# Kernel tuning notes

Hardware: AMD Instinct MI355X
Metric: run time of the kernel (lower is better)

The kernel has to match this reference:

```python
import jax, jax.numpy as jnp
import numpy as np

V_IPC, N_ROLES, D = 50000, 16, 256
B, L = 2048, 64
F_BIB, H1, H2, D_OUT = 512, 1024, 1024, 512
N_EXP, N_CLS = 8, 10
LN_EPS = 1e-5


def setup_inputs() -> dict:
    key = jax.random.key(0)
    ks = jax.random.split(key, 24)
    s = 0.05
    ipc_emb = jax.random.normal(ks[0], (V_IPC, D), jnp.float32) * s
    ipc_emb = ipc_emb.at[0].set(0.0)  # padding_idx=0
    role_emb = jax.random.normal(ks[1], (N_ROLES, D), jnp.float32) * s
    role_emb = role_emb.at[0].set(0.0)
    inp = {
        "ipc_indices": jax.random.randint(ks[2], (B, L), 0, V_IPC),
        "role_indices": jax.random.randint(ks[3], (B, L), 0, N_ROLES),
        "bibliometric_features": jax.random.normal(ks[4], (B, F_BIB), jnp.float32),
        "ipc_padding_mask": jax.random.randint(ks[5], (B, L), 0, 2).astype(jnp.int32),
        "top_k": 2,
        "ipc_emb": ipc_emb,
        "role_emb": role_emb,
        "Wq": jax.random.normal(ks[6], (D, D), jnp.float32) * s,
        "bq": jnp.zeros((D,), jnp.float32),
        "Wk": jax.random.normal(ks[7], (D, D), jnp.float32) * s,
        "bk": jnp.zeros((D,), jnp.float32),
        "Wv": jax.random.normal(ks[8], (D, D), jnp.float32) * s,
        "bv": jnp.zeros((D,), jnp.float32),
        "global_context": jax.random.normal(ks[9], (D,), jnp.float32) * s,
        "ln_g": jnp.ones((D,), jnp.float32),
        "ln_b": jnp.zeros((D,), jnp.float32),
        "gate_W": jax.random.normal(ks[10], (D, N_EXP), jnp.float32) * s,
        "gate_b": jnp.zeros((N_EXP,), jnp.float32),
        "expert_biases": jnp.zeros((N_EXP,), jnp.float32),
        "W1": jax.random.normal(ks[11], (N_EXP, F_BIB, H1), jnp.float32) * s,
        "b1": jnp.zeros((N_EXP, H1), jnp.float32),
        "W2": jax.random.normal(ks[12], (N_EXP, H1, H2), jnp.float32) * s,
        "b2": jnp.zeros((N_EXP, H2), jnp.float32),
        "W3": jax.random.normal(ks[13], (N_EXP, H2, D_OUT), jnp.float32) * s,
        "b3": jnp.zeros((N_EXP, D_OUT), jnp.float32),
        "head_W": jax.random.normal(ks[14], (D_OUT, N_CLS), jnp.float32) * s,
        "head_b": jnp.zeros((N_CLS,), jnp.float32),
    }
    return inp


def reference(ipc_indices, role_indices, bibliometric_features, ipc_padding_mask, top_k,
              ipc_emb, role_emb, Wq, bq, Wk, bk, Wv, bv, global_context, ln_g, ln_b,
              gate_W, gate_b, expert_biases, W1, b1, W2, b2, W3, b3, head_W, head_b):
    # embeddings + role combine  -> [B, L, D]
    x = ipc_emb[ipc_indices] + role_emb[role_indices]
    # attention pooling with a global learned query (same query for every batch row)
    keys = x @ Wk + bk                                  # [B, L, D]
    values = x @ Wv + bv                                # [B, L, D]
    q = global_context @ Wq + bq                        # [D]
    scores = jnp.einsum('d,bld->bl', q, keys)           # [B, L]
    scores = jnp.where(ipc_padding_mask == 0, -1e9, scores)
    attn = jax.nn.softmax(scores, axis=-1)              # [B, L]
    pooled = jnp.einsum('bl,bld->bd', attn, values)     # [B, D]
    mu = pooled.mean(-1, keepdims=True)
    var = ((pooled - mu) ** 2).mean(-1, keepdims=True)
    router_in = (pooled - mu) / jnp.sqrt(var + LN_EPS) * ln_g + ln_b
    # router: select with biased scores, gate with unbiased scores
    affinity = router_in @ gate_W + gate_b              # [B, E]
    sel_scores = affinity + expert_biases
    _, idx = jax.lax.top_k(sel_scores, top_k)           # [B, K]
    gw = jax.nn.softmax(jnp.take_along_axis(affinity, idx, axis=-1), axis=-1)  # [B, K]
    # dense all-expert MLP (reference form of masked per-expert loop)
    h = jax.nn.relu(jnp.einsum('bi,eih->ebh', bibliometric_features, W1) + b1[:, None, :])
    h = jax.nn.relu(jnp.einsum('ebh,ehj->ebj', h, W2) + b2[:, None, :])
    eo = jnp.einsum('ebj,ejo->ebo', h, W3) + b3[:, None, :]  # [E, B, O]
    # gather each token's top-k expert outputs and combine
    bidx = jnp.arange(idx.shape[0])[:, None]            # [B, 1]
    sel_out = eo[idx, bidx]                             # [B, K, O]
    moe_out = jnp.einsum('bk,bko->bo', gw, sel_out)     # [B, O]
    logits = moe_out @ head_W + head_b                  # [B, n_classes]
    return logits, idx
```

## Files before the change

### kernel.cpp

```cpp
#include <hip/hip_runtime.h>
#include <hip/hip_bf16.h>
#include <math.h>


#define LN_EPS 1e-5f

typedef __bf16 bf16_t;
typedef __bf16 bf16x8 __attribute__((ext_vector_type(8)));
typedef float f32x4 __attribute__((ext_vector_type(4)));

struct f4x2 { float4 a, b; };
__device__ __forceinline__ f4x2 ldA8(const float* p) {
  f4x2 v; v.a = *(const float4*)p; v.b = *(const float4*)(p + 4); return v;
}
__device__ __forceinline__ bf16x8 cvt8(const f4x2& v) {
  bf16x8 o;
  o[0] = (bf16_t)v.a.x; o[1] = (bf16_t)v.a.y; o[2] = (bf16_t)v.a.z; o[3] = (bf16_t)v.a.w;
  o[4] = (bf16_t)v.b.x; o[5] = (bf16_t)v.b.y; o[6] = (bf16_t)v.b.z; o[7] = (bf16_t)v.b.w;
  return o;
}

__global__ __launch_bounds__(256)
void transpose_prep(const float* __restrict__ W1, const float* __restrict__ W2,
                    const float* __restrict__ W3, bf16_t* __restrict__ B1,
                    bf16_t* __restrict__ B2, bf16_t* __restrict__ B3,
                    const float* __restrict__ Wq, const float* __restrict__ bq,
                    const float* __restrict__ Wk, const float* __restrict__ bk,
                    const float* __restrict__ gc, float* __restrict__ kq_out) {
  __shared__ float tile[64][65];
  const int z = blockIdx.z;
  if (z == 24) {
    if (blockIdx.y >= 2) return;
    float* q = &tile[0][0];
    float* red = &tile[0][0] + 256;
    const int t = threadIdx.x, bi = blockIdx.y * 16 + blockIdx.x;
    float s = bq[t];
    for (int d = 0; d < 256; d++) s += gc[d] * Wq[d * 256 + t];
    q[t] = s;
    __syncthreads();
    const int rl = t >> 5, sl = t & 31;
    const int r = bi * 8 + rl;
    float p = 0.f;
#pragma unroll
    for (int i = 0; i < 8; i++) { const int d = sl + 32 * i; p += Wk[r * 256 + d] * q[d]; }
#pragma unroll
    for (int o = 16; o > 0; o >>= 1) p += __shfl_down(p, o, 32);
    if (sl == 0) kq_out[r] = p;
    if (bi == 0) {
      float z2 = q[t] * bk[t];
      const int lane = t & 63, wave = t >> 6;
#pragma unroll
      for (int o = 32; o > 0; o >>= 1) z2 += __shfl_down(z2, o);
      if (lane == 0) red[wave] = z2;
      __syncthreads();
      if (t == 0) kq_out[256] = red[0] + red[1] + red[2] + red[3];
    }
    return;
  }
  const float* W; bf16_t* Bft; int K, N, e;
  if (z < 8)       { W = W1; Bft = B1; K = 512;  N = 1024; e = z; }
  else if (z < 16) { W = W2; Bft = B2; K = 1024; N = 1024; e = z - 8; }
  else             { W = W3; Bft = B3; K = 1024; N = 512;  e = z - 16; }
  const int n0 = blockIdx.x * 64, k0 = blockIdx.y * 64;
  if (n0 >= N || k0 >= K) return;
  const float* Wp = W + (size_t)e * K * N;
  bf16_t* Bp = Bft + (size_t)e * N * K;
  const int tq = threadIdx.x & 15, th = threadIdx.x >> 4;
#pragma unroll
  for (int i = 0; i < 4; i++) {
    const int row = th + 16 * i;
    *(float4*)&tile[row][tq * 4] = *(const float4*)(Wp + (size_t)(k0 + row) * N + n0 + tq * 4);
  }
  __syncthreads();
  const int lane = threadIdx.x & 63, sub = threadIdx.x >> 6;
  const int nk = K >> 5;
#pragma unroll
  for (int it = 0; it < 2; it++) {
    const int fid = sub + it * 4;
    const int ntl = fid & 3, ktl = fid >> 2;
    const int n_l = ntl * 16 + (lane & 15);
    const int k_l = ktl * 32 + (lane >> 4) * 8;
    bf16x8 o;
#pragma unroll
    for (int j = 0; j < 8; j++) o[j] = (bf16_t)tile[k_l + j][n_l];
    const size_t idx = ((((size_t)(n0 >> 4) + ntl) * nk + (k0 >> 5) + ktl) * 64 + lane) * 8;
    *(bf16x8*)(Bp + idx) = o;
  }
}

__global__ __launch_bounds__(256)
void score_tab_kernel(const float* __restrict__ ipc_emb,
                      const float* __restrict__ role_emb,
                      const float* __restrict__ kq_qbk, float* __restrict__ tab) {
  const int wave = threadIdx.x >> 6, lane = threadIdx.x & 63;
  const float4 kq = *(const float4*)(kq_qbk + lane * 4);
  const int base = (blockIdx.x * 4 + wave) * 32;
  for (int i = 0; i < 32; i++) {
    const int r = base + i;
    if (r >= 50016) return;
    const float* src = (r < 50000) ? (ipc_emb + (size_t)r * 256)
                                   : (role_emb + (size_t)(r - 50000) * 256);
    const float4 v = *(const float4*)(src + lane * 4);
    float p = v.x * kq.x + v.y * kq.y + v.z * kq.z + v.w * kq.w;
#pragma unroll
    for (int o = 32; o > 0; o >>= 1) p += __shfl_down(p, o);
    if (lane == 0) tab[r] = (r < 50000) ? p : (p + kq_qbk[256]);
  }
}

__global__ __launch_bounds__(256)
void xbar_kernel(const int* __restrict__ ipc_idx, const int* __restrict__ role_idx,
                 const int* __restrict__ maskp,
                 const float* __restrict__ ipc_emb, const float* __restrict__ role_emb,
                 const float* __restrict__ tab, float* __restrict__ xbar_g) {
  const int b = blockIdx.x;
  __shared__ float attn_s[64];
  __shared__ __align__(16) float part[4][256];
  const int t = threadIdx.x, wave = t >> 6, lane = t & 63;
  const int d0 = lane * 4;
  if (wave == 0) {
    const int ii = ipc_idx[b * 64 + lane], ri = role_idx[b * 64 + lane];
    float s = tab[ii] + tab[50000 + ri];
    s = (maskp[b * 64 + lane] == 0) ? -1e9f : s;
    float m = s;
#pragma unroll
    for (int o = 32; o > 0; o >>= 1) m = fmaxf(m, __shfl_xor(m, o));
    const float ev = expf(s - m);
    float sum = ev;
#pragma unroll
    for (int o = 32; o > 0; o >>= 1) sum += __shfl_xor(sum, o);
    attn_s[lane] = ev / sum;
  }
  __syncthreads();
  float p0 = 0.f, p1 = 0.f, p2 = 0.f, p3 = 0.f;
  for (int l = wave; l < 64; l += 4) {
    const float a = attn_s[l];
    if (a == 0.f) continue;
    const int ii = ipc_idx[b * 64 + l], ri = role_idx[b * 64 + l];
    const float4 xe = *(const float4*)(ipc_emb + (size_t)ii * 256 + d0);
    const float4 re = *(const float4*)(role_emb + (size_t)ri * 256 + d0);
    p0 += a * (xe.x + re.x); p1 += a * (xe.y + re.y);
    p2 += a * (xe.z + re.z); p3 += a * (xe.w + re.w);
  }
  *(float4*)&part[wave][d0] = make_float4(p0, p1, p2, p3);
  __syncthreads();
  xbar_g[(size_t)b * 256 + t] = part[0][t] + part[1][t] + part[2][t] + part[3][t];
}

__global__ __launch_bounds__(256)
void pool_kernel(const float* __restrict__ xbar_g, const float* __restrict__ Wv,
                 const float* __restrict__ bvec,
                 const float* __restrict__ ln_g, const float* __restrict__ ln_b,
                 const float* __restrict__ gate_W, const float* __restrict__ gate_b,
                 const float* __restrict__ expert_biases,
                 float* __restrict__ out_idx_f, int* __restrict__ ws_idx,
                 float* __restrict__ ws_gw) {
  const int rb = blockIdx.x * 8;
  __shared__ __align__(16) float xs[8][256];
  __shared__ __align__(16) float ps[8][260];
  const int t = threadIdx.x, wave = t >> 6, lane = t & 63;
  for (int i = t; i < 512; i += 256)
    ((float4*)xs)[i] = ((const float4*)(xbar_g + (size_t)rb * 256))[i];
  __syncthreads();
  const float* x0 = xs[wave * 2];
  const float* x1 = xs[wave * 2 + 1];
  f32x4 acc0 = {0.f, 0.f, 0.f, 0.f}, acc1 = {0.f, 0.f, 0.f, 0.f};
  for (int d = 0; d < 256; d += 4) {
    const float4 xa = *(const float4*)(x0 + d);
    const float4 xb = *(const float4*)(x1 + d);
#pragma unroll
    for (int j = 0; j < 4; j++) {
      const float4 wv = *(const float4*)(Wv + (size_t)(d + j) * 256 + lane * 4);
      const float aj = (&xa.x)[j], bj = (&xb.x)[j];
      acc0.x += aj * wv.x; acc0.y += aj * wv.y; acc0.z += aj * wv.z; acc0.w += aj * wv.w;
      acc1.x += bj * wv.x; acc1.y += bj * wv.y; acc1.z += bj * wv.z; acc1.w += bj * wv.w;
    }
  }
  const float4 bvv = *(const float4*)(bvec + lane * 4);
  acc0.x += bvv.x; acc0.y += bvv.y; acc0.z += bvv.z; acc0.w += bvv.w;
  acc1.x += bvv.x; acc1.y += bvv.y; acc1.z += bvv.z; acc1.w += bvv.w;
  *(f32x4*)&ps[wave * 2][lane * 4] = acc0;
  *(f32x4*)&ps[wave * 2 + 1][lane * 4] = acc1;
  __syncthreads();
  const float4 lg = *(const float4*)(ln_g + lane * 4);
  const float4 lb = *(const float4*)(ln_b + lane * 4);
#pragma unroll
  for (int rr = 0; rr < 2; rr++) {
    const int r = wave * 2 + rr;
    const float4 v = *(const float4*)&ps[r][lane * 4];
    float s1 = v.x + v.y + v.z + v.w;
#pragma unroll
    for (int o = 32; o > 0; o >>= 1) s1 += __shfl_xor(s1, o);
    const float mu = s1 * (1.f / 256.f);
    const float4 df = make_float4(v.x - mu, v.y - mu, v.z - mu, v.w - mu);
    float s2 = df.x * df.x + df.y * df.y + df.z * df.z + df.w * df.w;
#pragma unroll
    for (int o = 32; o > 0; o >>= 1) s2 += __shfl_xor(s2, o);
    const float inv = 1.f / sqrtf(s2 * (1.f / 256.f) + LN_EPS);
    f32x4 rv;
    rv[0] = df.x * inv * lg.x + lb.x; rv[1] = df.y * inv * lg.y + lb.y;
    rv[2] = df.z * inv * lg.z + lb.z; rv[3] = df.w * inv * lg.w + lb.w;
    f32x4 pa = {0.f, 0.f, 0.f, 0.f}, pb = {0.f, 0.f, 0.f, 0.f};
#pragma unroll
    for (int k = 0; k < 4; k++) {
      const int d = lane * 4 + k;
      const f32x4 g0 = *(const f32x4*)(gate_W + d * 8);
      const f32x4 g1 = *(const f32x4*)(gate_W + d * 8 + 4);
      pa += rv[k] * g0;
      pb += rv[k] * g1;
    }
#pragma unroll
    for (int o = 32; o > 0; o >>= 1) {
      pa[0] += __shfl_down(pa[0], o); pa[1] += __shfl_down(pa[1], o);
      pa[2] += __shfl_down(pa[2], o); pa[3] += __shfl_down(pa[3], o);
      pb[0] += __shfl_down(pb[0], o); pb[1] += __shfl_down(pb[1], o);
      pb[2] += __shfl_down(pb[2], o); pb[3] += __shfl_down(pb[3], o);
    }
    if (lane == 0) {
      float aff[8];
#pragma unroll
      for (int j = 0; j < 4; j++) { aff[j] = pa[j] + gate_b[j]; aff[4 + j] = pb[j] + gate_b[4 + j]; }
      float b0 = -1e30f; int i0 = 0;
#pragma unroll
      for (int j = 0; j < 8; j++) {
        const float s = aff[j] + expert_biases[j];
        if (s > b0) { b0 = s; i0 = j; }
      }
      float b1v = -1e30f; int i1 = 0;
#pragma unroll
      for (int j = 0; j < 8; j++) {
        const float s = aff[j] + expert_biases[j];
        if (j != i0 && s > b1v) { b1v = s; i1 = j; }
      }
      const float a0 = aff[i0], a1 = aff[i1];
      const float m = fmaxf(a0, a1);
      const float e0 = expf(a0 - m), e1 = expf(a1 - m);
      const float invs = 1.f / (e0 + e1);
      const int bg = rb + r;
      ws_idx[bg * 2] = i0; ws_idx[bg * 2 + 1] = i1;
      ws_gw[bg * 2] = e0 * invs; ws_gw[bg * 2 + 1] = e1 * invs;
      out_idx_f[bg * 2] = (float)i0; out_idx_f[bg * 2 + 1] = (float)i1;
    }
  }
}

__global__ __launch_bounds__(256)
void pack_kernel(const int* __restrict__ ws_idx, int* __restrict__ list_token,
                 int* __restrict__ a_of, int* __restrict__ offsets_g) {
  __shared__ int cnt[8]; __shared__ int off[9]; __shared__ int fill[8];
  const int t = threadIdx.x;
  if (t < 8) cnt[t] = 0;
  __syncthreads();
  for (int a = t; a < 4096; a += 256) atomicAdd(&cnt[ws_idx[a]], 1);
  __syncthreads();
  if (t == 0) {
    off[0] = 0;
    for (int e = 0; e < 8; e++) off[e + 1] = off[e] + ((cnt[e] + 63) & ~63);
  }
  __syncthreads();
  if (t < 8) fill[t] = off[t];
  if (t < 9) offsets_g[t] = off[t];
  for (int a = t; a < 4608; a += 256) list_token[a] = 0;
  __syncthreads();
  for (int a = t; a < 4096; a += 256) {
    const int e = ws_idx[a];
    const int pos = atomicAdd(&fill[e], 1);
    list_token[pos] = a >> 1;
    a_of[a] = pos;
  }
}

template <int NT, bool RELU>
__global__ __launch_bounds__(256)
void expert_gemm_g1(const float* __restrict__ bib, const int* __restrict__ list_token,
                    const bf16_t* __restrict__ Bft, const float* __restrict__ bias,
                    bf16_t* __restrict__ C, const int* __restrict__ offsets) {
  constexpr int K = 512, nk = K / 32;
  const int e = blockIdx.z;
  const int seg_hi = offsets[e + 1];
  const int blk_row = offsets[e] + blockIdx.y * 128;
  if (blk_row >= seg_hi) return;
  const int wave = threadIdx.x >> 6, lane = threadIdx.x & 63;
  const int row0 = blk_row + wave * 32;
  if (row0 >= seg_hi) return;
  const int n0 = blockIdx.x * 64;
  const int tok0 = list_token[row0 + (lane & 15)];
  const int tok1 = list_token[row0 + 16 + (lane & 15)];
  const float* Ap0 = bib + (size_t)tok0 * 512 + (lane >> 4) * 8;
  const float* Ap1 = bib + (size_t)tok1 * 512 + (lane >> 4) * 8;
  const bf16_t* Bp = Bft + (size_t)e * NT * K + ((size_t)(n0 >> 4) * nk * 512 + lane * 8);
  f32x4 acc[2][4];
#pragma unroll
  for (int i = 0; i < 2; i++)
#pragma unroll
    for (int j = 0; j < 4; j++) acc[i][j] = (f32x4){0.f, 0.f, 0.f, 0.f};
  f4x2 aS[2][2]; bf16x8 bX[2][4];
  aS[0][0] = ldA8(Ap0); aS[0][1] = ldA8(Ap1);
#pragma unroll
  for (int ni = 0; ni < 4; ni++) bX[0][ni] = *(const bf16x8*)(Bp + (size_t)ni * nk * 512);
#pragma unroll
  for (int kt = 0; kt < nk; kt++) {
    const int cur = kt & 1, nxt = cur ^ 1;
    if (kt + 1 < nk) {
      aS[nxt][0] = ldA8(Ap0 + (kt + 1) * 32);
      aS[nxt][1] = ldA8(Ap1 + (kt + 1) * 32);
#pragma unroll
      for (int ni = 0; ni < 4; ni++)
        bX[nxt][ni] = *(const bf16x8*)(Bp + ((size_t)ni * nk + kt + 1) * 512);
    }
    const bf16x8 a0 = cvt8(aS[cur][0]), a1 = cvt8(aS[cur][1]);
#pragma unroll
    for (int ni = 0; ni < 4; ni++) {
      acc[0][ni] = __builtin_amdgcn_mfma_f32_16x16x32_bf16(a0, bX[cur][ni], acc[0][ni], 0, 0, 0);
      acc[1][ni] = __builtin_amdgcn_mfma_f32_16x16x32_bf16(a1, bX[cur][ni], acc[1][ni], 0, 0, 0);
    }
  }
  const int fr = lane & 15, q = lane >> 4;
#pragma unroll
  for (int ni = 0; ni < 4; ni++) {
    const int col = n0 + ni * 16 + fr;
    const float bv = bias[e * NT + col];
#pragma unroll
    for (int mi = 0; mi < 2; mi++) {
#pragma unroll
      for (int r = 0; r < 4; r++) {
        const int row = row0 + mi * 16 + q * 4 + r;
        float v = acc[mi][ni][r] + bv;
        if (RELU) v = fmaxf(v, 0.f);
        C[(size_t)row * NT + col] = (bf16_t)v;
      }
    }
  }
}

template <int K, int NT, bool RELU, typename OUT_T>
__global__ __launch_bounds__(256)
void expert_gemm_ft(const bf16_t* __restrict__ A, const bf16_t* __restrict__ Bft,
                    const float* __restrict__ bias, OUT_T* __restrict__ C,
                    const int* __restrict__ offsets) {
  constexpr int nk = K / 32;
  const int e = blockIdx.z;
  const int seg_hi = offsets[e + 1];
  const int blk_row = offsets[e] + blockIdx.y * 128;
  if (blk_row >= seg_hi) return;
  const int wave = threadIdx.x >> 6, lane = threadIdx.x & 63;
  const int row0 = blk_row + wave * 32;
  if (row0 >= seg_hi) return;
  const int n0 = blockIdx.x * 64;
  const bf16_t* Ap = A + (size_t)(row0 + (lane & 15)) * K + ((lane >> 4) * 8);
  const bf16_t* Bp = Bft + (size_t)e * NT * K + ((size_t)(n0 >> 4) * nk * 512 + lane * 8);
  f32x4 acc[2][4];
#pragma unroll
  for (int i = 0; i < 2; i++)
#pragma unroll
    for (int j = 0; j < 4; j++) acc[i][j] = (f32x4){0.f, 0.f, 0.f, 0.f};
  bf16x8 aX[2][2], bX[2][4];
#pragma unroll
  for (int mi = 0; mi < 2; mi++) aX[0][mi] = *(const bf16x8*)(Ap + mi * 16 * K);
#pragma unroll
  for (int ni = 0; ni < 4; ni++) bX[0][ni] = *(const bf16x8*)(Bp + (size_t)ni * nk * 512);
#pragma unroll
  for (int kt = 0; kt < nk; kt++) {
    const int cur = kt & 1, nxt = cur ^ 1;
    if (kt + 1 < nk) {
#pragma unroll
      for (int mi = 0; mi < 2; mi++)
        aX[nxt][mi] = *(const bf16x8*)(Ap + mi * 16 * K + (kt + 1) * 32);
#pragma unroll
      for (int ni = 0; ni < 4; ni++)
        bX[nxt][ni] = *(const bf16x8*)(Bp + ((size_t)ni * nk + kt + 1) * 512);
    }
#pragma unroll
    for (int mi = 0; mi < 2; mi++)
#pragma unroll
      for (int ni = 0; ni < 4; ni++)
        acc[mi][ni] = __builtin_amdgcn_mfma_f32_16x16x32_bf16(aX[cur][mi], bX[cur][ni], acc[mi][ni], 0, 0, 0);
  }
  const int fr = lane & 15, q = lane >> 4;
#pragma unroll
  for (int ni = 0; ni < 4; ni++) {
    const int col = n0 + ni * 16 + fr;
    const float bv = bias[e * NT + col];
#pragma unroll
    for (int mi = 0; mi < 2; mi++) {
#pragma unroll
      for (int r = 0; r < 4; r++) {
        const int row = row0 + mi * 16 + q * 4 + r;
        float v = acc[mi][ni][r] + bv;
        if (RELU) v = fmaxf(v, 0.f);
        C[(size_t)row * NT + col] = (OUT_T)v;
      }
    }
  }
}

__global__ __launch_bounds__(256)
void head_kernel(const float* __restrict__ O, const int* __restrict__ a_of,
                 const float* __restrict__ ws_gw, const float* __restrict__ head_W,
                 const float* __restrict__ head_b, float* __restrict__ out) {
  const int b = blockIdx.x, t = threadIdx.x;
  __shared__ float m[512];
  const int a0 = a_of[b * 2], a1 = a_of[b * 2 + 1];
  const float g0 = ws_gw[b * 2], g1 = ws_gw[b * 2 + 1];
  for (int d = t; d < 512; d += 256)
    m[d] = g0 * O[(size_t)a0 * 512 + d] + g1 * O[(size_t)a1 * 512 + d];
  __syncthreads();
  if (t < 160) {
    const int c = t >> 4, ch = t & 15;
    float p = 0.f;
#pragma unroll
    for (int i = 0; i < 32; i++) {
      const int d = i * 16 + ch;
      p += m[d] * head_W[d * 10 + c];
    }
#pragma unroll
    for (int o = 8; o > 0; o >>= 1) p += __shfl_down(p, o, 16);
    if (ch == 0) out[b * 10 + c] = p + head_b[c];
  }
}

extern "C" void kernel_launch(void* const* d_in, const int* in_sizes, int n_in,
                              void* d_out, int out_size, void* d_ws, size_t ws_size,
                              hipStream_t stream) {
  const int* ipc_idx = (const int*)d_in[0];
  const int* role_idx = (const int*)d_in[1];
  const float* bib = (const float*)d_in[2];
  const int* maskp = (const int*)d_in[3];
  const float* ipc_emb = (const float*)d_in[5];
  const float* role_emb = (const float*)d_in[6];
  const float* Wq = (const float*)d_in[7];
  const float* bq = (const float*)d_in[8];
  const float* Wk = (const float*)d_in[9];
  const float* bk = (const float*)d_in[10];
  const float* Wv = (const float*)d_in[11];
  const float* bv = (const float*)d_in[12];
  const float* gc = (const float*)d_in[13];
  const float* ln_g = (const float*)d_in[14];
  const float* ln_b = (const float*)d_in[15];
  const float* gate_W = (const float*)d_in[16];
  const float* gate_b = (const float*)d_in[17];
  const float* exp_b = (const float*)d_in[18];
  const float* W1 = (const float*)d_in[19];
  const float* b1 = (const float*)d_in[20];
  const float* W2 = (const float*)d_in[21];
  const float* b2 = (const float*)d_in[22];
  const float* W3 = (const float*)d_in[23];
  const float* b3 = (const float*)d_in[24];
  const float* head_W = (const float*)d_in[25];
  const float* head_b = (const float*)d_in[26];

  char* ws = (char*)d_ws;
  size_t off = 0;
  auto alloc = [&](size_t bytes) -> char* {
    char* p = ws + off;
    off += (bytes + 255) & ~(size_t)255;
    return p;
  };
  float* kq_qbk = (float*)alloc(257 * 4);
  float* tab = (float*)alloc(50016 * 4);
  float* xbar_g = (float*)alloc((size_t)2048 * 256 * 4);
  int* ws_idx = (int*)alloc(4096 * 4);
  float* ws_gw = (float*)alloc(4096 * 4);
  int* list_tok = (int*)alloc(4608 * 4);
  int* a_of = (int*)alloc(4096 * 4);
  int* offs = (int*)alloc(9 * 4);
  bf16_t* W1t = (bf16_t*)alloc((size_t)8 * 1024 * 512 * 2);
  bf16_t* W2t = (bf16_t*)alloc((size_t)8 * 1024 * 1024 * 2);
  bf16_t* W3t = (bf16_t*)alloc((size_t)8 * 512 * 1024 * 2);
  bf16_t* H1c = (bf16_t*)alloc((size_t)4608 * 1024 * 2);
  bf16_t* H2c = (bf16_t*)alloc((size_t)4608 * 1024 * 2);
  float* Oc = (float*)alloc((size_t)4608 * 512 * 4);
  (void)in_sizes; (void)n_in; (void)out_size; (void)ws_size;

  float* out_logits = (float*)d_out;
  float* out_idx = (float*)d_out + 20480;

  transpose_prep<<<dim3(16, 16, 25), 256, 0, stream>>>(W1, W2, W3, W1t, W2t, W3t,
                                                       Wq, bq, Wk, bk, gc, kq_qbk);
  score_tab_kernel<<<391, 256, 0, stream>>>(ipc_emb, role_emb, kq_qbk, tab);
  xbar_kernel<<<2048, 256, 0, stream>>>(ipc_idx, role_idx, maskp, ipc_emb, role_emb,
                                        tab, xbar_g);
  pool_kernel<<<256, 256, 0, stream>>>(xbar_g, Wv, bv, ln_g, ln_b, gate_W, gate_b,
                                       exp_b, out_idx, ws_idx, ws_gw);
  pack_kernel<<<1, 256, 0, stream>>>(ws_idx, list_tok, a_of, offs);
  expert_gemm_g1<1024, true><<<dim3(16, 36, 8), 256, 0, stream>>>(bib, list_tok, W1t, b1, H1c, offs);
  expert_gemm_ft<1024, 1024, true, bf16_t><<<dim3(16, 36, 8), 256, 0, stream>>>(H1c, W2t, b2, H2c, offs);
  expert_gemm_ft<1024, 512, false, float><<<dim3(8, 36, 8), 256, 0, stream>>>(H2c, W3t, b3, Oc, offs);
  head_kernel<<<2048, 256, 0, stream>>>(Oc, a_of, ws_gw, head_W, head_b, out_logits);
}
```

Measured before the change: 379.7 us.

## Fold W3 into head weights, dropping the third expert GEMM

Since the last expert layer is linear and is followed directly by the linear head, W3·head_W and b3·head_W are precomputed per expert in the prep kernel, giving a 1024x10 matrix per expert. The head kernel then reads H2 rows directly and applies the folded weights. This removes the 1024x512 expert GEMM and the fp32 Oc intermediate. In exchange, the prep kernel recomputes the folded weights on every call, and the last layer now runs in fp32 from bf16 H2 rather than through a bf16 GEMM, which changes rounding slightly.

```diff
diff --git a/kernel.cpp b/kernel.cpp
--- a/kernel.cpp
+++ b/kernel.cpp
@@ -22,57 +22,106 @@
 
 __global__ __launch_bounds__(256)
 void transpose_prep(const float* __restrict__ W1, const float* __restrict__ W2,
-                    const float* __restrict__ W3, bf16_t* __restrict__ B1,
-                    bf16_t* __restrict__ B2, bf16_t* __restrict__ B3,
+                    bf16_t* __restrict__ B1, bf16_t* __restrict__ B2,
                     const float* __restrict__ Wq, const float* __restrict__ bq,
                     const float* __restrict__ Wk, const float* __restrict__ bk,
-                    const float* __restrict__ gc, float* __restrict__ kq_out) {
+                    const float* __restrict__ gc, float* __restrict__ kq_out,
+                    const float* __restrict__ W3, const float* __restrict__ head_W,
+                    const float* __restrict__ b3, float* __restrict__ W3hT,
+                    float* __restrict__ b3h) {
   __shared__ float tile[64][65];
   const int z = blockIdx.z;
-  if (z == 24) {
-    if (blockIdx.y >= 2) return;
-    float* q = &tile[0][0];
-    float* red = &tile[0][0] + 256;
-    const int t = threadIdx.x, bi = blockIdx.y * 16 + blockIdx.x;
-    float s = bq[t];
-    for (int d = 0; d < 256; d++) s += gc[d] * Wq[d * 256 + t];
-    q[t] = s;
+  const int t = threadIdx.x;
+  if (z == 16) {
+    if (blockIdx.y < 2) {
+      float* q = &tile[0][0];
+      float* red = &tile[0][0] + 256;
+      const int bi = blockIdx.y * 16 + blockIdx.x;
+      float s = bq[t];
+      for (int d = 0; d < 256; d++) s += gc[d] * Wq[d * 256 + t];
+      q[t] = s;
+      __syncthreads();
+      const int rl = t >> 5, sl = t & 31;
+      const int r = bi * 8 + rl;
+      float p = 0.f;
+#pragma unroll
+      for (int i = 0; i < 8; i++) { const int d = sl + 32 * i; p += Wk[r * 256 + d] * q[d]; }
+#pragma unroll
+      for (int o = 16; o > 0; o >>= 1) p += __shfl_down(p, o, 32);
+      if (sl == 0) kq_out[r] = p;
+      if (bi == 0) {
+        float z2 = q[t] * bk[t];
+        const int lane = t & 63, wave = t >> 6;
+#pragma unroll
+        for (int o = 32; o > 0; o >>= 1) z2 += __shfl_down(z2, o);
+        if (lane == 0) red[wave] = z2;
+        __syncthreads();
+        if (t == 0) kq_out[256] = red[0] + red[1] + red[2] + red[3];
+      }
+    } else if (blockIdx.y == 2 && blockIdx.x < 8) {
+      float* red = &tile[0][0];
+      const int e = blockIdx.x;
+      const int c = t & 15, chunk = t >> 4;
+      float p = 0.f;
+      if (c < 10) {
+        for (int o = chunk * 32; o < chunk * 32 + 32; o++)
+          p += b3[e * 512 + o] * head_W[o * 10 + c];
+      }
+      red[chunk * 16 + c] = p;
+      __syncthreads();
+      if (t < 10) {
+        float s = 0.f;
+#pragma unroll
+        for (int ch = 0; ch < 16; ch++) s += red[ch * 16 + t];
+        b3h[e * 10 + t] = s;
+      }
+    }
+    return;
+  }
+  if (z >= 17) {
+    float* red = &tile[0][0];
+    const int blk = (z - 17) * 256 + blockIdx.y * 16 + blockIdx.x;
+    const int j_local = t >> 4, sub = t & 15;
+    const int g = blk * 16 + j_local;
+    const int e = g >> 10, j = g & 1023;
+    const float* wrow = W3 + ((size_t)e * 1024 + j) * 512 + sub * 32;
+    const float* hw = head_W + sub * 32 * 10;
+    float acc[10];
+#pragma unroll
+    for (int c = 0; c < 10; c++) acc[c] = 0.f;
+    for (int o = 0; o < 32; o++) {
+      const float w = wrow[o];
+#pragma unroll
+      for (int c = 0; c < 10; c++) acc[c] += w * hw[o * 10 + c];
+    }
+#pragma unroll
+    for (int c = 0; c < 10; c++) red[(j_local * 16 + sub) * 10 + c] = acc[c];
     __syncthreads();
-    const int rl = t >> 5, sl = t & 31;
-    const int r = bi * 8 + rl;
-    float p = 0.f;
-#pragma unroll
-    for (int i = 0; i < 8; i++) { const int d = sl + 32 * i; p += Wk[r * 256 + d] * q[d]; }
-#pragma unroll
-    for (int o = 16; o > 0; o >>= 1) p += __shfl_down(p, o, 32);
-    if (sl == 0) kq_out[r] = p;
-    if (bi == 0) {
-      float z2 = q[t] * bk[t];
-      const int lane = t & 63, wave = t >> 6;
-#pragma unroll
-      for (int o = 32; o > 0; o >>= 1) z2 += __shfl_down(z2, o);
-      if (lane == 0) red[wave] = z2;
-      __syncthreads();
-      if (t == 0) kq_out[256] = red[0] + red[1] + red[2] + red[3];
+    if (t < 160) {
+      const int jl = t / 10, c = t - jl * 10;
+      float s = 0.f;
+#pragma unroll
+      for (int ss = 0; ss < 16; ss++) s += red[(jl * 16 + ss) * 10 + c];
+      const int gg = blk * 16 + jl;
+      W3hT[((size_t)(gg >> 10) * 10 + c) * 1024 + (gg & 1023)] = s;
     }
     return;
   }
   const float* W; bf16_t* Bft; int K, N, e;
-  if (z < 8)       { W = W1; Bft = B1; K = 512;  N = 1024; e = z; }
-  else if (z < 16) { W = W2; Bft = B2; K = 1024; N = 1024; e = z - 8; }
-  else             { W = W3; Bft = B3; K = 1024; N = 512;  e = z - 16; }
+  if (z < 8) { W = W1; Bft = B1; K = 512;  N = 1024; e = z; }
+  else       { W = W2; Bft = B2; K = 1024; N = 1024; e = z - 8; }
   const int n0 = blockIdx.x * 64, k0 = blockIdx.y * 64;
   if (n0 >= N || k0 >= K) return;
   const float* Wp = W + (size_t)e * K * N;
   bf16_t* Bp = Bft + (size_t)e * N * K;
-  const int tq = threadIdx.x & 15, th = threadIdx.x >> 4;
+  const int tq = t & 15, th = t >> 4;
 #pragma unroll
   for (int i = 0; i < 4; i++) {
     const int row = th + 16 * i;
     *(float4*)&tile[row][tq * 4] = *(const float4*)(Wp + (size_t)(k0 + row) * N + n0 + tq * 4);
   }
   __syncthreads();
-  const int lane = threadIdx.x & 63, sub = threadIdx.x >> 6;
+  const int lane = t & 63, sub = t >> 6;
   const int nk = K >> 5;
 #pragma unroll
   for (int it = 0; it < 2; it++) {
@@ -395,27 +444,47 @@
 }
 
 __global__ __launch_bounds__(256)
-void head_kernel(const float* __restrict__ O, const int* __restrict__ a_of,
-                 const float* __restrict__ ws_gw, const float* __restrict__ head_W,
-                 const float* __restrict__ head_b, float* __restrict__ out) {
+void head2_kernel(const bf16_t* __restrict__ H2, const int* __restrict__ a_of,
+                  const int* __restrict__ ws_idx, const float* __restrict__ ws_gw,
+                  const float* __restrict__ W3hT, const float* __restrict__ b3h,
+                  const float* __restrict__ head_b, float* __restrict__ out) {
   const int b = blockIdx.x, t = threadIdx.x;
-  __shared__ float m[512];
+  __shared__ float m[2][1024];
+  __shared__ float partial[2][10];
   const int a0 = a_of[b * 2], a1 = a_of[b * 2 + 1];
+  const int e0 = ws_idx[b * 2], e1 = ws_idx[b * 2 + 1];
   const float g0 = ws_gw[b * 2], g1 = ws_gw[b * 2 + 1];
-  for (int d = t; d < 512; d += 256)
-    m[d] = g0 * O[(size_t)a0 * 512 + d] + g1 * O[(size_t)a1 * 512 + d];
+  {
+    const int k = t >> 7, dd = (t & 127) * 8;
+    const int row = k ? a1 : a0;
+    const bf16x8 v = *(const bf16x8*)(H2 + (size_t)row * 1024 + dd);
+#pragma unroll
+    for (int j = 0; j < 8; j++) m[k][dd + j] = (float)v[j];
+  }
   __syncthreads();
   if (t < 160) {
-    const int c = t >> 4, ch = t & 15;
+    const int sub = t & 7;
+    const int pc = t >> 3;
+    const int k = pc >= 10;
+    const int c = k ? pc - 10 : pc;
+    const int e = k ? e1 : e0;
+    const float* wrow = W3hT + ((size_t)e * 10 + c) * 1024 + sub * 128;
+    const float* mm = m[k] + sub * 128;
     float p = 0.f;
 #pragma unroll
-    for (int i = 0; i < 32; i++) {
-      const int d = i * 16 + ch;
-      p += m[d] * head_W[d * 10 + c];
-    }
-#pragma unroll
-    for (int o = 8; o > 0; o >>= 1) p += __shfl_down(p, o, 16);
-    if (ch == 0) out[b * 10 + c] = p + head_b[c];
+    for (int i = 0; i < 128; i += 4) {
+      const float4 a = *(const float4*)(mm + i);
+      const float4 w = *(const float4*)(wrow + i);
+      p += a.x * w.x + a.y * w.y + a.z * w.z + a.w * w.w;
+    }
+#pragma unroll
+    for (int o = 4; o > 0; o >>= 1) p += __shfl_down(p, o, 8);
+    if (sub == 0) partial[k][c] = p;
+  }
+  __syncthreads();
+  if (t < 10) {
+    out[b * 10 + t] = g0 * (partial[0][t] + b3h[e0 * 10 + t])
+                    + g1 * (partial[1][t] + b3h[e1 * 10 + t]) + head_b[t];
   }
 }
 
@@ -466,17 +535,17 @@
   int* offs = (int*)alloc(9 * 4);
   bf16_t* W1t = (bf16_t*)alloc((size_t)8 * 1024 * 512 * 2);
   bf16_t* W2t = (bf16_t*)alloc((size_t)8 * 1024 * 1024 * 2);
-  bf16_t* W3t = (bf16_t*)alloc((size_t)8 * 512 * 1024 * 2);
+  float* W3hT = (float*)alloc((size_t)8 * 10 * 1024 * 4);
+  float* b3h = (float*)alloc(80 * 4);
   bf16_t* H1c = (bf16_t*)alloc((size_t)4608 * 1024 * 2);
   bf16_t* H2c = (bf16_t*)alloc((size_t)4608 * 1024 * 2);
-  float* Oc = (float*)alloc((size_t)4608 * 512 * 4);
   (void)in_sizes; (void)n_in; (void)out_size; (void)ws_size;
 
   float* out_logits = (float*)d_out;
   float* out_idx = (float*)d_out + 20480;
 
-  transpose_prep<<<dim3(16, 16, 25), 256, 0, stream>>>(W1, W2, W3, W1t, W2t, W3t,
-                                                       Wq, bq, Wk, bk, gc, kq_qbk);
+  transpose_prep<<<dim3(16, 16, 19), 256, 0, stream>>>(
+      W1, W2, W1t, W2t, Wq, bq, Wk, bk, gc, kq_qbk, W3, head_W, b3, W3hT, b3h);
   score_tab_kernel<<<391, 256, 0, stream>>>(ipc_emb, role_emb, kq_qbk, tab);
   xbar_kernel<<<2048, 256, 0, stream>>>(ipc_idx, role_idx, maskp, ipc_emb, role_emb,
                                         tab, xbar_g);
@@ -485,6 +554,6 @@
   pack_kernel<<<1, 256, 0, stream>>>(ws_idx, list_tok, a_of, offs);
   expert_gemm_g1<1024, true><<<dim3(16, 36, 8), 256, 0, stream>>>(bib, list_tok, W1t, b1, H1c, offs);
   expert_gemm_ft<1024, 1024, true, bf16_t><<<dim3(16, 36, 8), 256, 0, stream>>>(H1c, W2t, b2, H2c, offs);
-  expert_gemm_ft<1024, 512, false, float><<<dim3(8, 36, 8), 256, 0, stream>>>(H2c, W3t, b3, Oc, offs);
-  head_kernel<<<2048, 256, 0, stream>>>(Oc, a_of, ws_gw, head_W, head_b, out_logits);
-}
+  head2_kernel<<<2048, 256, 0, stream>>>(H2c, a_of, ws_idx, ws_gw, W3hT, b3h,
+                                         head_b, out_logits);
+}
```

Result: no change. 382.8 us (+0.8%).
